# Optimization experiments

Hardware: AMD Instinct MI355X
Metric: run time of the kernel (lower is better)

## Reference

```python
import jax, jax.numpy as jnp
import numpy as np

EMB = 64      # embedding_dim
HID = 128     # hidden_dim
SCALE = 4.0   # InputEmbedding scale
N_TRACKS = 32768


def lstm_cell(x, h, c, W_ih, W_hh, b_ih, b_hh):
    # torch.nn.LSTMCell gate order: i, f, g, o
    gates = x @ W_ih.T + b_ih + h @ W_hh.T + b_hh  # [N, 4*HID]
    i, f, g, o = jnp.split(gates, 4, axis=-1)
    i = jax.nn.sigmoid(i)
    f = jax.nn.sigmoid(f)
    g = jnp.tanh(g)
    o = jax.nn.sigmoid(o)
    c_new = f * c + i * g
    h_new = o * jnp.tanh(c_new)
    return h_new, c_new


def setup_inputs() -> dict:
    key = jax.random.key(0)
    ks = jax.random.split(key, 14)

    def init(k, shape, fan_in):
        b = 1.0 / np.sqrt(fan_in)
        return jax.random.uniform(k, shape, jnp.float32, -b, b)

    return {
        "observed": jax.random.normal(ks[0], (9, N_TRACKS, 2), jnp.float32),
        "prediction": jax.random.normal(ks[1], (12, N_TRACKS, 2), jnp.float32),
        # InputEmbedding: Linear(2, EMB-2) followed by ReLU, 2 tag dims appended
        "W_emb": init(ks[2], (EMB - 2, 2), 2),
        "b_emb": init(ks[3], (EMB - 2,), 2),
        # LSTMCell(EMB, HID)
        "W_ih": init(ks[4], (4 * HID, EMB), HID),
        "W_hh": init(ks[5], (4 * HID, HID), HID),
        "b_ih": init(ks[6], (4 * HID,), HID),
        "b_hh": init(ks[7], (4 * HID,), HID),
        # real_classifier MLP: 128 -> 64 -> 32 -> 1, ReLU after each Linear
        "W1": init(ks[8], (HID // 2, HID), HID),
        "b1": init(ks[9], (HID // 2,), HID),
        "W2": init(ks[10], (HID // 4, HID // 2), HID // 2),
        "b2": init(ks[11], (HID // 4,), HID // 2),
        "W3": init(ks[12], (1, HID // 4), HID // 4),
        "b3": init(ks[13], (1,), HID // 4),
    }


def reference(observed, prediction, W_emb, b_emb, W_ih, W_hh, b_ih, b_hh,
              W1, b1, W2, b2, W3, b3):
    seq = jnp.concatenate([observed, prediction], axis=0)  # [T, N, 2]
    N = seq.shape[1]
    h = jnp.zeros((N, HID), seq.dtype)
    c = jnp.zeros((N, HID), seq.dtype)

    # tag_step: start_enc tag is one-hot at position EMB-2
    tag = jnp.zeros((N, EMB), seq.dtype).at[:, EMB - 2].set(1.0)
    h, c = lstm_cell(tag, h, c, W_ih, W_hh, b_ih, b_hh)

    def step(carry, xs):
        h, c = carry
        obs1, obs2 = xs
        # track visible iff both frames are non-NaN
        mask = ~(jnp.isnan(obs1[:, 0]) | jnp.isnan(obs2[:, 0]))  # [N]
        vel = jnp.where(mask[:, None], obs2 - obs1, 0.0)
        emb = jax.nn.relu((vel * SCALE) @ W_emb.T + b_emb)       # [N, EMB-2]
        emb = jnp.concatenate([emb, jnp.zeros((N, 2), emb.dtype)], axis=1)
        h_new, c_new = lstm_cell(emb, h, c, W_ih, W_hh, b_ih, b_hh)
        # scatter updated states back only for visible tracks
        h = jnp.where(mask[:, None], h_new, h)
        c = jnp.where(mask[:, None], c_new, c)
        return (h, c), None

    (h, c), _ = jax.lax.scan(step, (h, c), (seq[:-1], seq[1:]))

    # real_classifier applied to hidden state of track 0
    x = jax.nn.relu(h[0] @ W1.T + b1)
    x = jax.nn.relu(x @ W2.T + b2)
    scores = jax.nn.relu(x @ W3.T + b3)  # shape (1,)
    return scores
```

## Files before the change

kernel.cpp:

```cpp
#include <hip/hip_runtime.h>
#include <math.h>

#define NT 32768
#define SCALEF 4.0f
#define WSIG 0x57AB0000u
#define GSIG 0x6B3C0000u

typedef _Float16 h2v __attribute__((ext_vector_type(2)));
typedef unsigned uvec4 __attribute__((ext_vector_type(4)));

__device__ __forceinline__ unsigned pk2(float lo, float hi) {
    unsigned a = (unsigned)__builtin_bit_cast(unsigned short, (_Float16)lo);
    unsigned b = (unsigned)__builtin_bit_cast(unsigned short, (_Float16)hi);
    return a | (b << 16);
}
__device__ __forceinline__ float upk_lo(unsigned u) {
    return (float)__builtin_bit_cast(_Float16, (unsigned short)(u & 0xffffu));
}
__device__ __forceinline__ float upk_hi(unsigned u) {
    return (float)__builtin_bit_cast(_Float16, (unsigned short)(u >> 16));
}
__device__ __forceinline__ float dot2(unsigned w, unsigned h, float acc) {
#if defined(__has_builtin) && __has_builtin(__builtin_amdgcn_fdot2)
    return __builtin_amdgcn_fdot2(__builtin_bit_cast(h2v, w),
                                  __builtin_bit_cast(h2v, h), acc, false);
#else
    float r = fmaf(upk_lo(w), upk_lo(h), acc);
    return fmaf(upk_hi(w), upk_hi(h), r);
#endif
}
__device__ __forceinline__ float tanhfast(float x) {
    return 1.0f - 2.0f * __builtin_amdgcn_rcpf(1.0f + __expf(2.0f * x));
}
__device__ __forceinline__ float frame_val(const float* __restrict__ obs,
                                           const float* __restrict__ pred,
                                           int F, int d) {
    return (F < 9) ? obs[F * (NT * 2) + d] : pred[(F - 9) * (NT * 2) + d];
}

__device__ __forceinline__ int rof2(int k2row) {
    int t = k2row & 255, slot = k2row >> 8;
    int lane = t & 63, wv = t >> 6;
    return (lane & 3) * 128 + wv * 16 + (lane >> 2) + slot * 64;
}

#define QBCAST(dst, src, CTRL)                                                  \
    dst = __int_as_float(__builtin_amdgcn_update_dpp(                           \
        0, __float_as_int(src), (CTRL), 0xF, 0xF, true))

#define PIN16(a0,a1,a2,a3,a4,a5,a6,a7,a8,a9,a10,a11,a12,a13,a14,a15)            \
    asm("" : "+v"(a0), "+v"(a1), "+v"(a2),  "+v"(a3),  "+v"(a4),  "+v"(a5),     \
             "+v"(a6), "+v"(a7), "+v"(a8),  "+v"(a9),  "+v"(a10), "+v"(a11),    \
             "+v"(a12), "+v"(a13), "+v"(a14), "+v"(a15))

__attribute__((amdgpu_waves_per_eu(1, 1)))
__global__ void __launch_bounds__(256) lstm_fused(
    const float* __restrict__ observed, const float* __restrict__ prediction,
    const float* __restrict__ W_emb,    const float* __restrict__ b_emb,
    const float* __restrict__ W_ih,     const float* __restrict__ W_hh,
    const float* __restrict__ b_ih,     const float* __restrict__ b_hh,
    const float* __restrict__ W1, const float* __restrict__ b1,
    const float* __restrict__ W2, const float* __restrict__ b2,
    const float* __restrict__ W3, const float* __restrict__ b3,
    unsigned* __restrict__ wsgx, uvec4* __restrict__ wsw,
    unsigned* __restrict__ flags, float* __restrict__ out)
{
    const int tid = (int)threadIdx.x;

    if (blockIdx.x < 8) {
        const int b = (int)blockIdx.x;
        __shared__ float    velx[21], vely[21];
        __shared__ unsigned xs_pk[21 * 32];
        __shared__ unsigned wih_pk[64 * 32];
        __shared__ float    bias64[64];

        for (int task = tid; task < 512; task += 256) {
            int row = task >> 3, seg = task & 7;
            int k2row = b * 64 + row;
            int t = k2row & 255, slot = k2row >> 8;
            int r = rof2(k2row);
            const float4* src = reinterpret_cast<const float4*>(W_hh) + r * 32 + seg * 4;
            float4 a0 = src[0], a1 = src[1], a2 = src[2], a3 = src[3];
            uvec4 u0, u1;
            u0.x = pk2(a0.x, a0.y); u0.y = pk2(a0.z, a0.w);
            u0.z = pk2(a1.x, a1.y); u0.w = pk2(a1.z, a1.w);
            u1.x = pk2(a2.x, a2.y); u1.y = pk2(a2.z, a2.w);
            u1.z = pk2(a3.x, a3.y); u1.w = pk2(a3.z, a3.w);
            wsw[(slot * 16 + seg * 2 + 0) * 256 + t] = u0;
            wsw[(slot * 16 + seg * 2 + 1) * 256 + t] = u1;
        }
        __syncthreads();
        if (tid == 0) {
            __threadfence();
            __hip_atomic_store(&flags[b], WSIG + b, __ATOMIC_RELEASE, __HIP_MEMORY_SCOPE_AGENT);
        }

        for (int task = tid; task < 512; task += 256) {
            int row = task >> 3, seg = task & 7;
            int r = rof2(b * 64 + row);
            const float4* src = reinterpret_cast<const float4*>(W_ih) + r * 16 + seg * 2;
            float4 a0 = src[0], a1 = src[1];
            wih_pk[row * 32 + (((seg * 4 + 0) + row) & 31)] = pk2(a0.x, a0.y);
            wih_pk[row * 32 + (((seg * 4 + 1) + row) & 31)] = pk2(a0.z, a0.w);
            wih_pk[row * 32 + (((seg * 4 + 2) + row) & 31)] = pk2(a1.x, a1.y);
            wih_pk[row * 32 + (((seg * 4 + 3) + row) & 31)] = pk2(a1.z, a1.w);
            if (seg == 0) bias64[row] = b_ih[r] + b_hh[r];
        }
        if (tid < 20) {
            float ax = frame_val(observed, prediction, tid,     0);
            float ay = frame_val(observed, prediction, tid,     1);
            float bx = frame_val(observed, prediction, tid + 1, 0);
            float by = frame_val(observed, prediction, tid + 1, 1);
            unsigned ua = __float_as_uint(ax) & 0x7fffffffu;
            unsigned ub = __float_as_uint(bx) & 0x7fffffffu;
            bool m = !((ua > 0x7f800000u) || (ub > 0x7f800000u));
            velx[tid + 1] = m ? (bx - ax) * SCALEF : 0.0f;
            vely[tid + 1] = m ? (by - ay) * SCALEF : 0.0f;
        }
        if (tid == 20) { velx[0] = 0.0f; vely[0] = 0.0f; }
        __syncthreads();

        unsigned short* xs16 = (unsigned short*)xs_pk;
        for (int idx = tid; idx < 21 * 64; idx += 256) {
            int s = idx >> 6, e = idx & 63;
            float v;
            if (s == 0)      v = (e == 62) ? 1.0f : 0.0f;
            else if (e < 62) v = fmaxf(velx[s] * W_emb[2 * e] + vely[s] * W_emb[2 * e + 1] + b_emb[e], 0.0f);
            else             v = 0.0f;
            xs16[s * 64 + e] = __builtin_bit_cast(unsigned short, (_Float16)v);
        }
        __syncthreads();

        unsigned short* gx16 = (unsigned short*)wsgx;
        for (int task = tid; task < 21 * 64; task += 256) {
            int s = task >> 6, lr = task & 63;
            int k2row = b * 64 + lr;
            int t = k2row & 255, slot = k2row >> 8;
            float acc;
            if (s == 0) {
                acc = bias64[lr] + upk_lo(wih_pk[lr * 32 + ((31 + lr) & 31)]);
            } else {
                float a0 = bias64[lr], a1 = 0.0f;
                #pragma unroll
                for (int q = 0; q < 32; q += 2) {
                    a0 = dot2(wih_pk[lr * 32 + ((q + lr) & 31)],     xs_pk[s * 32 + q],     a0);
                    a1 = dot2(wih_pk[lr * 32 + ((q + 1 + lr) & 31)], xs_pk[s * 32 + q + 1], a1);
                }
                acc = a0 + a1;
            }
            gx16[s * 512 + t * 2 + slot] = __builtin_bit_cast(unsigned short, (_Float16)acc);
        }
        __syncthreads();
        if (tid == 0) {
            __threadfence();
            __hip_atomic_store(&flags[8 + b], GSIG + b, __ATOMIC_RELEASE, __HIP_MEMORY_SCOPE_AGENT);
        }
        return;
    }

    const int lane = tid & 63;
    const int wv   = tid >> 6;
    const int g    = lane & 3;
    const int uA   = wv * 16 + (lane >> 2);
    const int uB   = uA + 64;

    __shared__ unsigned gxl[21 * 256];
    __shared__ uvec4    hqb[2][16];
    __shared__ float    hfin[128], mlp1[64], mlp2[32];

    bool mb = true;
    if (lane >= 1 && lane <= 20) {
        float ax = frame_val(observed, prediction, lane - 1, 0);
        float bx = frame_val(observed, prediction, lane,     0);
        unsigned ua = __float_as_uint(ax) & 0x7fffffffu;
        unsigned ub = __float_as_uint(bx) & 0x7fffffffu;
        mb = !((ua > 0x7f800000u) || (ub > 0x7f800000u));
    }
    unsigned mbits = (unsigned)(__ballot(lane < 21 && mb) & 0x1FFFFFull);

    #pragma unroll 1
    while (__hip_atomic_load(&flags[wv], __ATOMIC_ACQUIRE,
                             __HIP_MEMORY_SCOPE_AGENT) != WSIG + (unsigned)wv) {}
    uvec4 w0  = wsw[ 0 * 256 + tid], w1  = wsw[ 1 * 256 + tid];
    uvec4 w2  = wsw[ 2 * 256 + tid], w3  = wsw[ 3 * 256 + tid];
    uvec4 w4  = wsw[ 4 * 256 + tid], w5  = wsw[ 5 * 256 + tid];
    uvec4 w6  = wsw[ 6 * 256 + tid], w7  = wsw[ 7 * 256 + tid];
    uvec4 w8  = wsw[ 8 * 256 + tid], w9  = wsw[ 9 * 256 + tid];
    uvec4 w10 = wsw[10 * 256 + tid], w11 = wsw[11 * 256 + tid];
    uvec4 w12 = wsw[12 * 256 + tid], w13 = wsw[13 * 256 + tid];
    uvec4 w14 = wsw[14 * 256 + tid], w15 = wsw[15 * 256 + tid];

    #pragma unroll 1
    while (__hip_atomic_load(&flags[4 + wv], __ATOMIC_ACQUIRE,
                             __HIP_MEMORY_SCOPE_AGENT) != WSIG + 4u + (unsigned)wv) {}
    uvec4 v0  = wsw[16 * 256 + tid], v1  = wsw[17 * 256 + tid];
    uvec4 v2  = wsw[18 * 256 + tid], v3  = wsw[19 * 256 + tid];
    uvec4 v4  = wsw[20 * 256 + tid], v5  = wsw[21 * 256 + tid];
    uvec4 v6  = wsw[22 * 256 + tid], v7  = wsw[23 * 256 + tid];
    uvec4 v8  = wsw[24 * 256 + tid], v9  = wsw[25 * 256 + tid];
    uvec4 v10 = wsw[26 * 256 + tid], v11 = wsw[27 * 256 + tid];
    uvec4 v12 = wsw[28 * 256 + tid], v13 = wsw[29 * 256 + tid];
    uvec4 v14 = wsw[30 * 256 + tid], v15 = wsw[31 * 256 + tid];

    #pragma unroll 1
    while (__hip_atomic_load(&flags[8 + wv], __ATOMIC_ACQUIRE,
                             __HIP_MEMORY_SCOPE_AGENT) != GSIG + (unsigned)wv) {}
    #pragma unroll 1
    while (__hip_atomic_load(&flags[12 + wv], __ATOMIC_ACQUIRE,
                             __HIP_MEMORY_SCOPE_AGENT) != GSIG + 4u + (unsigned)wv) {}
    #pragma unroll
    for (int i = 0; i < 21; ++i) gxl[i * 256 + tid] = wsgx[i * 256 + tid];

    const float sc = (g == 2) ? 2.0f : -1.0f;
    float cA = 0.0f, cB = 0.0f, hA = 0.0f, hB = 0.0f;
    int cur = 0;

#define STEP_TAIL(preA, preB)                                                   \
    {                                                                           \
        float eA  = __expf(sc * (preA));                                        \
        float rcA = __builtin_amdgcn_rcpf(1.0f + eA);                           \
        float actA = (g == 2) ? fmaf(-2.0f, rcA, 1.0f) : rcA;                   \
        float eB  = __expf(sc * (preB));                                        \
        float rcB = __builtin_amdgcn_rcpf(1.0f + eB);                           \
        float actB = (g == 2) ? fmaf(-2.0f, rcB, 1.0f) : rcB;                   \
        float giA, gfA, ggA, goA, giB, gfB, ggB, goB;                           \
        QBCAST(giA, actA, 0x00); QBCAST(gfA, actA, 0x55);                       \
        QBCAST(ggA, actA, 0xAA); QBCAST(goA, actA, 0xFF);                       \
        QBCAST(giB, actB, 0x00); QBCAST(gfB, actB, 0x55);                       \
        QBCAST(ggB, actB, 0xAA); QBCAST(goB, actB, 0xFF);                       \
        cA = fmaf(gfA, cA, giA * ggA);  hA = goA * tanhfast(cA);                \
        cB = fmaf(gfB, cB, giB * ggB);  hB = goB * tanhfast(cB);                \
        if ((lane & 3) == 0) {                                                  \
            unsigned short* hw = (unsigned short*)&hqb[cur ^ 1][0];             \
            hw[uA] = __builtin_bit_cast(unsigned short, (_Float16)hA);          \
            hw[uB] = __builtin_bit_cast(unsigned short, (_Float16)hB);          \
        }                                                                       \
        __syncthreads();                                                        \
        cur ^= 1;                                                               \
    }

    {
        unsigned gp = gxl[tid];
        STEP_TAIL(upk_lo(gp), upk_hi(gp));
    }

#define G4B(K, WK, VK)                                                          \
    {                                                                           \
        uvec4 hv = hqb[cur][K];                                                 \
        aA0 = dot2(WK.x, hv.x, aA0); aA1 = dot2(WK.y, hv.y, aA1);               \
        aA0 = dot2(WK.z, hv.z, aA0); aA1 = dot2(WK.w, hv.w, aA1);               \
        aB0 = dot2(VK.x, hv.x, aB0); aB1 = dot2(VK.y, hv.y, aB1);               \
        aB0 = dot2(VK.z, hv.z, aB0); aB1 = dot2(VK.w, hv.w, aB1);               \
    }

    #pragma unroll 1
    for (int s = 1; s < 21; ++s) {
        if (mbits & (1u << s)) {
            PIN16(w0,w1,w2,w3,w4,w5,w6,w7,w8,w9,w10,w11,w12,w13,w14,w15);
            PIN16(v0,v1,v2,v3,v4,v5,v6,v7,v8,v9,v10,v11,v12,v13,v14,v15);
            unsigned gp = gxl[s * 256 + tid];
            float aA0 = 0.0f, aA1 = 0.0f, aB0 = 0.0f, aB1 = 0.0f;
            G4B( 0, w0,  v0)  G4B( 1, w1,  v1)  G4B( 2, w2,  v2)  G4B( 3, w3,  v3)
            G4B( 4, w4,  v4)  G4B( 5, w5,  v5)  G4B( 6, w6,  v6)  G4B( 7, w7,  v7)
            G4B( 8, w8,  v8)  G4B( 9, w9,  v9)  G4B(10, w10, v10) G4B(11, w11, v11)
            G4B(12, w12, v12) G4B(13, w13, v13) G4B(14, w14, v14) G4B(15, w15, v15)
            float preA = (aA0 + aA1) + upk_lo(gp);
            float preB = (aB0 + aB1) + upk_hi(gp);
            STEP_TAIL(preA, preB);
        }
    }

    if ((lane & 3) == 0) { hfin[uA] = hA; hfin[uB] = hB; }
    __syncthreads();
    if (tid < 64) {
        const float4* W1r = reinterpret_cast<const float4*>(W1 + tid * 128);
        float a = b1[tid];
        #pragma unroll
        for (int q = 0; q < 32; ++q) {
            float4 w = W1r[q];
            a = fmaf(w.x, hfin[4*q], a);   a = fmaf(w.y, hfin[4*q+1], a);
            a = fmaf(w.z, hfin[4*q+2], a); a = fmaf(w.w, hfin[4*q+3], a);
        }
        mlp1[tid] = fmaxf(a, 0.0f);
    }
    __syncthreads();
    if (tid < 32) {
        const float4* W2r = reinterpret_cast<const float4*>(W2 + tid * 64);
        float a = b2[tid];
        #pragma unroll
        for (int q = 0; q < 16; ++q) {
            float4 w = W2r[q];
            a = fmaf(w.x, mlp1[4*q], a);   a = fmaf(w.y, mlp1[4*q+1], a);
            a = fmaf(w.z, mlp1[4*q+2], a); a = fmaf(w.w, mlp1[4*q+3], a);
        }
        mlp2[tid] = fmaxf(a, 0.0f);
    }
    __syncthreads();
    if (tid == 0) {
        float a = b3[0];
        #pragma unroll
        for (int k = 0; k < 32; ++k) a += W3[k] * mlp2[k];
        out[0] = fmaxf(a, 0.0f);
    }
}

extern "C" void kernel_launch(void* const* d_in, const int* in_sizes, int n_in,
                              void* d_out, int out_size, void* d_ws, size_t ws_size,
                              hipStream_t stream) {
    unsigned* wsgx  = (unsigned*)d_ws;
    uvec4*    wsw   = (uvec4*)((char*)d_ws + 32768);
    unsigned* flags = (unsigned*)((char*)d_ws + 196608);
    lstm_fused<<<dim3(9), dim3(256), 0, stream>>>(
        (const float*)d_in[0],  (const float*)d_in[1],
        (const float*)d_in[2],  (const float*)d_in[3],
        (const float*)d_in[4],  (const float*)d_in[5],
        (const float*)d_in[6],  (const float*)d_in[7],
        (const float*)d_in[8],  (const float*)d_in[9],
        (const float*)d_in[10], (const float*)d_in[11],
        (const float*)d_in[12], (const float*)d_in[13],
        wsgx, wsw, flags, (float*)d_out);
}
```

Before: 98.11 us.

## Hoist global loads, compute tag step locally, overlap with producer blocks

The producer blocks now issue all their global loads (W_hh, W_ih, embedding weights, biases, frames) up front instead of in serial loops, so memory latencies overlap. The consumer block computes the initial tag-step gates directly from W_ih column 62 and the biases, then runs the first LSTM step before waiting on the producer flags, hiding part of the handoff latency. It also prefetches the MLP weights into L2 ahead of use and switches exp to a native exp2 with the log2(e) factor folded into the scale. The cost is more registers held live and some redundant loads, and the tag-step gates are now computed in fp32 rather than from the fp16-packed values.

Result: no change. 98.03 us (-0.1%).

```diff
diff --git a/kernel.cpp b/kernel.cpp
--- a/kernel.cpp
+++ b/kernel.cpp
@@ -5,6 +5,7 @@
 #define SCALEF 4.0f
 #define WSIG 0x57AB0000u
 #define GSIG 0x6B3C0000u
+#define L2E 1.4426950408889634f
 
 typedef _Float16 h2v __attribute__((ext_vector_type(2)));
 typedef unsigned uvec4 __attribute__((ext_vector_type(4)));
@@ -29,8 +30,15 @@
     return fmaf(upk_hi(w), upk_hi(h), r);
 #endif
 }
+__device__ __forceinline__ float exp2fast(float x) {
+#if defined(__has_builtin) && __has_builtin(__builtin_amdgcn_exp2f)
+    return __builtin_amdgcn_exp2f(x);
+#else
+    return __builtin_exp2f(x);
+#endif
+}
 __device__ __forceinline__ float tanhfast(float x) {
-    return 1.0f - 2.0f * __builtin_amdgcn_rcpf(1.0f + __expf(2.0f * x));
+    return 1.0f - 2.0f * __builtin_amdgcn_rcpf(1.0f + exp2fast(x * (2.0f * L2E)));
 }
 __device__ __forceinline__ float frame_val(const float* __restrict__ obs,
                                            const float* __restrict__ pred,
@@ -74,20 +82,47 @@
         __shared__ unsigned wih_pk[64 * 32];
         __shared__ float    bias64[64];
 
-        for (int task = tid; task < 512; task += 256) {
-            int row = task >> 3, seg = task & 7;
-            int k2row = b * 64 + row;
-            int t = k2row & 255, slot = k2row >> 8;
-            int r = rof2(k2row);
-            const float4* src = reinterpret_cast<const float4*>(W_hh) + r * 32 + seg * 4;
-            float4 a0 = src[0], a1 = src[1], a2 = src[2], a3 = src[3];
+        const int row0 = tid >> 3, seg = tid & 7;
+        const int row1 = row0 + 32;
+        const int rr0 = rof2(b * 64 + row0);
+        const int rr1 = rof2(b * 64 + row1);
+        const float4* s0 = reinterpret_cast<const float4*>(W_hh) + rr0 * 32 + seg * 4;
+        const float4* s1 = reinterpret_cast<const float4*>(W_hh) + rr1 * 32 + seg * 4;
+        float4 h00 = s0[0], h01 = s0[1], h02 = s0[2], h03 = s0[3];
+        float4 h10 = s1[0], h11 = s1[1], h12 = s1[2], h13 = s1[3];
+        const float4* i0 = reinterpret_cast<const float4*>(W_ih) + rr0 * 16 + seg * 2;
+        const float4* i1 = reinterpret_cast<const float4*>(W_ih) + rr1 * 16 + seg * 2;
+        float4 a00 = i0[0], a01 = i0[1];
+        float4 a10 = i1[0], a11 = i1[1];
+        const int ec = (tid & 63) < 62 ? (tid & 63) : 61;
+        float we0 = W_emb[2 * ec], we1 = W_emb[2 * ec + 1], be = b_emb[ec];
+        float bi = 0.0f, bh = 0.0f;
+        if (tid < 64) { int rb = rof2(b * 64 + tid); bi = b_ih[rb]; bh = b_hh[rb]; }
+        float fax = 0.0f, fay = 0.0f, fbx = 0.0f, fby = 0.0f;
+        if (tid < 20) {
+            fax = frame_val(observed, prediction, tid,     0);
+            fay = frame_val(observed, prediction, tid,     1);
+            fbx = frame_val(observed, prediction, tid + 1, 0);
+            fby = frame_val(observed, prediction, tid + 1, 1);
+        }
+
+        {
+            int t0 = (b * 64 + row0) & 255, sl0 = (b * 64 + row0) >> 8;
             uvec4 u0, u1;
-            u0.x = pk2(a0.x, a0.y); u0.y = pk2(a0.z, a0.w);
-            u0.z = pk2(a1.x, a1.y); u0.w = pk2(a1.z, a1.w);
-            u1.x = pk2(a2.x, a2.y); u1.y = pk2(a2.z, a2.w);
-            u1.z = pk2(a3.x, a3.y); u1.w = pk2(a3.z, a3.w);
-            wsw[(slot * 16 + seg * 2 + 0) * 256 + t] = u0;
-            wsw[(slot * 16 + seg * 2 + 1) * 256 + t] = u1;
+            u0.x = pk2(h00.x, h00.y); u0.y = pk2(h00.z, h00.w);
+            u0.z = pk2(h01.x, h01.y); u0.w = pk2(h01.z, h01.w);
+            u1.x = pk2(h02.x, h02.y); u1.y = pk2(h02.z, h02.w);
+            u1.z = pk2(h03.x, h03.y); u1.w = pk2(h03.z, h03.w);
+            wsw[(sl0 * 16 + seg * 2 + 0) * 256 + t0] = u0;
+            wsw[(sl0 * 16 + seg * 2 + 1) * 256 + t0] = u1;
+            int t1 = (b * 64 + row1) & 255, sl1 = (b * 64 + row1) >> 8;
+            uvec4 u2, u3;
+            u2.x = pk2(h10.x, h10.y); u2.y = pk2(h10.z, h10.w);
+            u2.z = pk2(h11.x, h11.y); u2.w = pk2(h11.z, h11.w);
+            u3.x = pk2(h12.x, h12.y); u3.y = pk2(h12.z, h12.w);
+            u3.z = pk2(h13.x, h13.y); u3.w = pk2(h13.z, h13.w);
+            wsw[(sl1 * 16 + seg * 2 + 0) * 256 + t1] = u2;
+            wsw[(sl1 * 16 + seg * 2 + 1) * 256 + t1] = u3;
         }
         __syncthreads();
         if (tid == 0) {
@@ -95,27 +130,21 @@
             __hip_atomic_store(&flags[b], WSIG + b, __ATOMIC_RELEASE, __HIP_MEMORY_SCOPE_AGENT);
         }
 
-        for (int task = tid; task < 512; task += 256) {
-            int row = task >> 3, seg = task & 7;
-            int r = rof2(b * 64 + row);
-            const float4* src = reinterpret_cast<const float4*>(W_ih) + r * 16 + seg * 2;
-            float4 a0 = src[0], a1 = src[1];
-            wih_pk[row * 32 + (((seg * 4 + 0) + row) & 31)] = pk2(a0.x, a0.y);
-            wih_pk[row * 32 + (((seg * 4 + 1) + row) & 31)] = pk2(a0.z, a0.w);
-            wih_pk[row * 32 + (((seg * 4 + 2) + row) & 31)] = pk2(a1.x, a1.y);
-            wih_pk[row * 32 + (((seg * 4 + 3) + row) & 31)] = pk2(a1.z, a1.w);
-            if (seg == 0) bias64[row] = b_ih[r] + b_hh[r];
-        }
+        wih_pk[row0 * 32 + (((seg * 4 + 0) + row0) & 31)] = pk2(a00.x, a00.y);
+        wih_pk[row0 * 32 + (((seg * 4 + 1) + row0) & 31)] = pk2(a00.z, a00.w);
+        wih_pk[row0 * 32 + (((seg * 4 + 2) + row0) & 31)] = pk2(a01.x, a01.y);
+        wih_pk[row0 * 32 + (((seg * 4 + 3) + row0) & 31)] = pk2(a01.z, a01.w);
+        wih_pk[row1 * 32 + (((seg * 4 + 0) + row1) & 31)] = pk2(a10.x, a10.y);
+        wih_pk[row1 * 32 + (((seg * 4 + 1) + row1) & 31)] = pk2(a10.z, a10.w);
+        wih_pk[row1 * 32 + (((seg * 4 + 2) + row1) & 31)] = pk2(a11.x, a11.y);
+        wih_pk[row1 * 32 + (((seg * 4 + 3) + row1) & 31)] = pk2(a11.z, a11.w);
+        if (tid < 64) bias64[tid] = bi + bh;
         if (tid < 20) {
-            float ax = frame_val(observed, prediction, tid,     0);
-            float ay = frame_val(observed, prediction, tid,     1);
-            float bx = frame_val(observed, prediction, tid + 1, 0);
-            float by = frame_val(observed, prediction, tid + 1, 1);
-            unsigned ua = __float_as_uint(ax) & 0x7fffffffu;
-            unsigned ub = __float_as_uint(bx) & 0x7fffffffu;
+            unsigned ua = __float_as_uint(fax) & 0x7fffffffu;
+            unsigned ub = __float_as_uint(fbx) & 0x7fffffffu;
             bool m = !((ua > 0x7f800000u) || (ub > 0x7f800000u));
-            velx[tid + 1] = m ? (bx - ax) * SCALEF : 0.0f;
-            vely[tid + 1] = m ? (by - ay) * SCALEF : 0.0f;
+            velx[tid + 1] = m ? (fbx - fax) * SCALEF : 0.0f;
+            vely[tid + 1] = m ? (fby - fay) * SCALEF : 0.0f;
         }
         if (tid == 20) { velx[0] = 0.0f; vely[0] = 0.0f; }
         __syncthreads();
@@ -125,7 +154,7 @@
             int s = idx >> 6, e = idx & 63;
             float v;
             if (s == 0)      v = (e == 62) ? 1.0f : 0.0f;
-            else if (e < 62) v = fmaxf(velx[s] * W_emb[2 * e] + vely[s] * W_emb[2 * e + 1] + b_emb[e], 0.0f);
+            else if (e < 62) v = fmaxf(velx[s] * we0 + vely[s] * we1 + be, 0.0f);
             else             v = 0.0f;
             xs16[s * 64 + e] = __builtin_bit_cast(unsigned short, (_Float16)v);
         }
@@ -168,6 +197,13 @@
     __shared__ uvec4    hqb[2][16];
     __shared__ float    hfin[128], mlp1[64], mlp2[32];
 
+    const int rA = rof2(tid), rB = rof2(256 + tid);
+    float g0A = b_ih[rA] + b_hh[rA] + W_ih[rA * 64 + 62];
+    float g0B = b_ih[rB] + b_hh[rB] + W_ih[rB * 64 + 62];
+    float pf = W1[tid * 32];
+    if (tid < 64) pf += W2[tid * 32];
+    if (tid == 0) pf += W3[0] + b1[0] + b1[32] + b2[0] + b3[0];
+
     bool mb = true;
     if (lane >= 1 && lane <= 20) {
         float ax = frame_val(observed, prediction, lane - 1, 0);
@@ -178,49 +214,16 @@
     }
     unsigned mbits = (unsigned)(__ballot(lane < 21 && mb) & 0x1FFFFFull);
 
-    #pragma unroll 1
-    while (__hip_atomic_load(&flags[wv], __ATOMIC_ACQUIRE,
-                             __HIP_MEMORY_SCOPE_AGENT) != WSIG + (unsigned)wv) {}
-    uvec4 w0  = wsw[ 0 * 256 + tid], w1  = wsw[ 1 * 256 + tid];
-    uvec4 w2  = wsw[ 2 * 256 + tid], w3  = wsw[ 3 * 256 + tid];
-    uvec4 w4  = wsw[ 4 * 256 + tid], w5  = wsw[ 5 * 256 + tid];
-    uvec4 w6  = wsw[ 6 * 256 + tid], w7  = wsw[ 7 * 256 + tid];
-    uvec4 w8  = wsw[ 8 * 256 + tid], w9  = wsw[ 9 * 256 + tid];
-    uvec4 w10 = wsw[10 * 256 + tid], w11 = wsw[11 * 256 + tid];
-    uvec4 w12 = wsw[12 * 256 + tid], w13 = wsw[13 * 256 + tid];
-    uvec4 w14 = wsw[14 * 256 + tid], w15 = wsw[15 * 256 + tid];
-
-    #pragma unroll 1
-    while (__hip_atomic_load(&flags[4 + wv], __ATOMIC_ACQUIRE,
-                             __HIP_MEMORY_SCOPE_AGENT) != WSIG + 4u + (unsigned)wv) {}
-    uvec4 v0  = wsw[16 * 256 + tid], v1  = wsw[17 * 256 + tid];
-    uvec4 v2  = wsw[18 * 256 + tid], v3  = wsw[19 * 256 + tid];
-    uvec4 v4  = wsw[20 * 256 + tid], v5  = wsw[21 * 256 + tid];
-    uvec4 v6  = wsw[22 * 256 + tid], v7  = wsw[23 * 256 + tid];
-    uvec4 v8  = wsw[24 * 256 + tid], v9  = wsw[25 * 256 + tid];
-    uvec4 v10 = wsw[26 * 256 + tid], v11 = wsw[27 * 256 + tid];
-    uvec4 v12 = wsw[28 * 256 + tid], v13 = wsw[29 * 256 + tid];
-    uvec4 v14 = wsw[30 * 256 + tid], v15 = wsw[31 * 256 + tid];
-
-    #pragma unroll 1
-    while (__hip_atomic_load(&flags[8 + wv], __ATOMIC_ACQUIRE,
-                             __HIP_MEMORY_SCOPE_AGENT) != GSIG + (unsigned)wv) {}
-    #pragma unroll 1
-    while (__hip_atomic_load(&flags[12 + wv], __ATOMIC_ACQUIRE,
-                             __HIP_MEMORY_SCOPE_AGENT) != GSIG + 4u + (unsigned)wv) {}
-    #pragma unroll
-    for (int i = 0; i < 21; ++i) gxl[i * 256 + tid] = wsgx[i * 256 + tid];
-
-    const float sc = (g == 2) ? 2.0f : -1.0f;
+    const float scl = (g == 2) ? (2.0f * L2E) : (-L2E);
     float cA = 0.0f, cB = 0.0f, hA = 0.0f, hB = 0.0f;
     int cur = 0;
 
 #define STEP_TAIL(preA, preB)                                                   \
     {                                                                           \
-        float eA  = __expf(sc * (preA));                                        \
+        float eA  = exp2fast(scl * (preA));                                     \
         float rcA = __builtin_amdgcn_rcpf(1.0f + eA);                           \
         float actA = (g == 2) ? fmaf(-2.0f, rcA, 1.0f) : rcA;                   \
-        float eB  = __expf(sc * (preB));                                        \
+        float eB  = exp2fast(scl * (preB));                                     \
         float rcB = __builtin_amdgcn_rcpf(1.0f + eB);                           \
         float actB = (g == 2) ? fmaf(-2.0f, rcB, 1.0f) : rcB;                   \
         float giA, gfA, ggA, goA, giB, gfB, ggB, goB;                           \
@@ -239,10 +242,41 @@
         cur ^= 1;                                                               \
     }
 
-    {
-        unsigned gp = gxl[tid];
-        STEP_TAIL(upk_lo(gp), upk_hi(gp));
-    }
+    STEP_TAIL(g0A, g0B);
+    asm volatile("" :: "v"(pf));
+
+    #pragma unroll 1
+    while (__hip_atomic_load(&flags[wv], __ATOMIC_ACQUIRE,
+                             __HIP_MEMORY_SCOPE_AGENT) != WSIG + (unsigned)wv) {}
+    uvec4 w0  = wsw[ 0 * 256 + tid], w1  = wsw[ 1 * 256 + tid];
+    uvec4 w2  = wsw[ 2 * 256 + tid], w3  = wsw[ 3 * 256 + tid];
+    uvec4 w4  = wsw[ 4 * 256 + tid], w5  = wsw[ 5 * 256 + tid];
+    uvec4 w6  = wsw[ 6 * 256 + tid], w7  = wsw[ 7 * 256 + tid];
+    uvec4 w8  = wsw[ 8 * 256 + tid], w9  = wsw[ 9 * 256 + tid];
+    uvec4 w10 = wsw[10 * 256 + tid], w11 = wsw[11 * 256 + tid];
+    uvec4 w12 = wsw[12 * 256 + tid], w13 = wsw[13 * 256 + tid];
+    uvec4 w14 = wsw[14 * 256 + tid], w15 = wsw[15 * 256 + tid];
+
+    #pragma unroll 1
+    while (__hip_atomic_load(&flags[4 + wv], __ATOMIC_ACQUIRE,
+                             __HIP_MEMORY_SCOPE_AGENT) != WSIG + 4u + (unsigned)wv) {}
+    uvec4 v0  = wsw[16 * 256 + tid], v1  = wsw[17 * 256 + tid];
+    uvec4 v2  = wsw[18 * 256 + tid], v3  = wsw[19 * 256 + tid];
+    uvec4 v4  = wsw[20 * 256 + tid], v5  = wsw[21 * 256 + tid];
+    uvec4 v6  = wsw[22 * 256 + tid], v7  = wsw[23 * 256 + tid];
+    uvec4 v8  = wsw[24 * 256 + tid], v9  = wsw[25 * 256 + tid];
+    uvec4 v10 = wsw[26 * 256 + tid], v11 = wsw[27 * 256 + tid];
+    uvec4 v12 = wsw[28 * 256 + tid], v13 = wsw[29 * 256 + tid];
+    uvec4 v14 = wsw[30 * 256 + tid], v15 = wsw[31 * 256 + tid];
+
+    #pragma unroll 1
+    while (__hip_atomic_load(&flags[8 + wv], __ATOMIC_ACQUIRE,
+                             __HIP_MEMORY_SCOPE_AGENT) != GSIG + (unsigned)wv) {}
+    #pragma unroll 1
+    while (__hip_atomic_load(&flags[12 + wv], __ATOMIC_ACQUIRE,
+                             __HIP_MEMORY_SCOPE_AGENT) != GSIG + 4u + (unsigned)wv) {}
+    #pragma unroll
+    for (int i = 1; i < 21; ++i) gxl[i * 256 + tid] = wsgx[i * 256 + tid];
 
 #define G4B(K, WK, VK)                                                          \
     {                                                                           \
```
